# Performance work log

Hardware: AMD Instinct MI355X
Metric: run time of the kernel (lower is better)

The kernel has to match this reference:

```python
import jax, jax.numpy as jnp
import numpy as np

EPS = 1e-5
SCALE = 1.0 / np.float32(np.sqrt(64.0))  # 1/sqrt(d_Q)


def layernorm(x):
    # fresh nn.LayerNorm each call: gamma=1, beta=0
    m = jnp.mean(x, axis=-1, keepdims=True)
    v = jnp.mean((x - m) ** 2, axis=-1, keepdims=True)
    return (x - m) * jax.lax.rsqrt(v + EPS)


def setup_inputs() -> dict:
    key = jax.random.key(0)
    ks = jax.random.split(key, 8)
    B, S, D, H, F = 32, 512, 256, 64, 256
    w = 0.05
    return {
        "x": jax.random.normal(ks[0], (B, S, D), jnp.float32),
        "mask": jax.random.randint(ks[1], (B, 6, S, S), 0, 2).astype(jnp.int32),
        "Wq": jax.random.normal(ks[2], (6, D, H), jnp.float32) * w,
        "Wk": jax.random.normal(ks[3], (6, D, H), jnp.float32) * w,
        "Wv": jax.random.normal(ks[4], (6, D, H), jnp.float32) * w,
        "Wfc": jax.random.normal(ks[5], (6, H, D), jnp.float32) * w,
        "W1": jax.random.normal(ks[6], (D, F), jnp.float32) * w,
        "W2": jax.random.normal(ks[7], (F, D), jnp.float32) * w,
    }


def reference(x, mask, Wq, Wk, Wv, Wfc, W1, W2):
    m = mask.astype(bool)                                   # [B,6,S,S]
    # batched over the 6 relation branches (r axis)
    Q = jnp.einsum('bsd,rdh->brsh', x, Wq)                  # [B,6,S,64]
    K = jnp.einsum('bsd,rdh->brsh', x, Wk)
    V = jnp.einsum('bsd,rdh->brsh', x, Wv)
    score = jnp.einsum('brsh,brth->brst', Q, K) * SCALE     # [B,6,S,S]
    score = jnp.where(m, jnp.float32(-1e9), score)
    attn = jax.nn.softmax(score, axis=-1)
    attn = jnp.where(m, jnp.float32(0.0), attn)             # post-softmax zeroing
    ctx = jnp.einsum('brst,brth->brsh', attn, V)            # [B,6,S,64]
    proj = jnp.einsum('brsh,rhd->brsd', ctx, Wfc)           # [B,6,S,256]
    branch = layernorm(proj + x[:, None, :, :])             # residual + fresh LN per branch
    s = jnp.sum(branch, axis=1)                             # sum of 6 branches [B,S,256]
    ffn = jnp.maximum(jnp.einsum('bsd,df->bsf', s, W1), 0.0)
    ffn = jnp.einsum('bsf,fd->bsd', ffn, W2)
    return layernorm(ffn + s)
```

## Files before the change

kernel.cpp:

```cpp
#include <hip/hip_runtime.h>
#include <hip/hip_bf16.h>

#define BB 32
#define RR 6
#define SS 512
#define DD 256
#define HH 64
#define FF 256

typedef short  short8 __attribute__((ext_vector_type(8)));
typedef short  short4v __attribute__((ext_vector_type(4)));
typedef float  f32x4  __attribute__((ext_vector_type(4)));
typedef unsigned short ushort_t;
typedef unsigned int   uint_t;

__device__ __forceinline__ ushort_t f2bf(float f) {
    __hip_bfloat16 b = __float2bfloat16(f);
    return __builtin_bit_cast(ushort_t, b);
}
__device__ __forceinline__ float bf2f(ushort_t u) {
    return __bfloat162float(__builtin_bit_cast(__hip_bfloat16, u));
}

__global__ __launch_bounds__(256) void convert_all_kernel(
        const float* __restrict__ x,
        const float* __restrict__ Wq, const float* __restrict__ Wk, const float* __restrict__ Wv,
        const float* __restrict__ Wfc, const float* __restrict__ W1, const float* __restrict__ W2,
        ushort_t* __restrict__ xb, ushort_t* __restrict__ wT, ushort_t* __restrict__ w1T,
        ushort_t* __restrict__ w2T, ushort_t* __restrict__ wfcT) {
    int bid = blockIdx.x;
    if (bid < 4096) {
        int gid = bid * 256 + threadIdx.x;
        float4 fv = ((const float4*)x)[gid];
        short4v o;
        o[0] = (short)f2bf(fv.x); o[1] = (short)f2bf(fv.y);
        o[2] = (short)f2bf(fv.z); o[3] = (short)f2bf(fv.w);
        *(short4v*)(xb + (size_t)gid * 4) = o;
        return;
    }
    int gid = (bid - 4096) * 256 + threadIdx.x;
    if (gid < 294912) {
        int n = gid >> 8, d = gid & 255;
        int r = n / 192, rem = n % 192;
        int which = rem >> 6, h = rem & 63;
        const float* W = which == 0 ? Wq : which == 1 ? Wk : Wv;
        wT[gid] = f2bf(W[(size_t)r * DD * HH + (size_t)d * HH + h]);
    } else if (gid < 360448) {
        int gg = gid - 294912;
        int f = gg >> 8, d = gg & 255;
        w1T[gg] = f2bf(W1[(size_t)d * FF + f]);
    } else if (gid < 425984) {
        int gg = gid - 360448;
        int d = gg >> 8, f = gg & 255;
        w2T[gg] = f2bf(W2[(size_t)f * DD + d]);
    } else {
        int gg = gid - 425984;
        int n = gg >> 6, h = gg & 63;
        int r = n >> 8, d = n & 255;
        wfcT[gg] = f2bf(Wfc[((size_t)r * HH + h) * DD + d]);
    }
}

__global__ __launch_bounds__(256) void qkv_mfma_kernel(
        const ushort_t* __restrict__ xb, const ushort_t* __restrict__ wT,
        ushort_t* __restrict__ q, ushort_t* __restrict__ k, ushort_t* __restrict__ v) {
    int bid = blockIdx.x;
    int id = (bid & 7) * 288 + (bid >> 3);
    int rt = id / 18, cw = id % 18;
    int r = cw / 3, which = cw % 3;

    int tid = threadIdx.x;
    int wv = tid >> 6, l = tid & 63;
    int wr = wv >> 1, wc = wv & 1;
    int g = l >> 4, lc = l & 15;

    const ushort_t* Arow = xb + ((size_t)(rt * 128 + wr * 64 + lc)) * DD + g * 8;
    const ushort_t* Brow = wT + ((size_t)(cw * 64 + wc * 32 + lc)) * DD + g * 8;

    f32x4 acc[4][2] = {};
    #pragma unroll 4
    for (int ks = 0; ks < 8; ++ks) {
        short8 af[4], bf[2];
        #pragma unroll
        for (int m = 0; m < 4; ++m)
            af[m] = *(const short8*)(Arow + (size_t)m * 16 * DD + ks * 32);
        #pragma unroll
        for (int n = 0; n < 2; ++n)
            bf[n] = *(const short8*)(Brow + (size_t)n * 16 * DD + ks * 32);
        #pragma unroll
        for (int m = 0; m < 4; ++m)
            #pragma unroll
            for (int n = 0; n < 2; ++n)
                acc[m][n] = __builtin_amdgcn_mfma_f32_16x16x32_bf16(af[m], bf[n], acc[m][n], 0, 0, 0);
    }

    ushort_t* outb = which == 0 ? q : which == 1 ? k : v;
    #pragma unroll
    for (int m = 0; m < 4; ++m) {
        #pragma unroll
        for (int reg = 0; reg < 4; ++reg) {
            int grow = rt * 128 + wr * 64 + m * 16 + g * 4 + reg;
            int orow = ((grow >> 9) * RR + r) * SS + (grow & (SS - 1));
            #pragma unroll
            for (int n = 0; n < 2; ++n)
                outb[(size_t)orow * HH + wc * 32 + n * 16 + lc] = f2bf(acc[m][n][reg]);
        }
    }
}

__global__ __launch_bounds__(256) void attn_mfma_kernel(
        const ushort_t* __restrict__ q, const ushort_t* __restrict__ k,
        const ushort_t* __restrict__ v, const int* __restrict__ mask,
        ushort_t* __restrict__ ctx) {
    int wg = blockIdx.x;
    int id = (wg & 7) * 192 + (wg >> 3);
    int br = id >> 3, qt = id & 7;

    __shared__ ushort_t K_lds[64 * 72];
    __shared__ ushort_t VT_lds[64 * 66];
    __shared__ ushort_t P_lds[4][16 * 72];

    int tid = threadIdx.x;
    int wv = tid >> 6, l = tid & 63;
    int g = l >> 4, lc = l & 15;

    int q0 = qt * 64 + wv * 16;
    const size_t base_kv = (size_t)br * SS * HH;

    short8 qf[2];
    #pragma unroll
    for (int kk = 0; kk < 2; ++kk)
        qf[kk] = *(const short8*)(q + ((size_t)br * SS + q0 + lc) * HH + kk * 32 + g * 8);

    f32x4 O[4] = {{0,0,0,0},{0,0,0,0},{0,0,0,0},{0,0,0,0}};
    float lrun[4] = {0.f, 0.f, 0.f, 0.f};

    const int* mb = mask + ((size_t)br * SS + q0) * SS;

    for (int t0 = 0; t0 < SS; t0 += 64) {
        __syncthreads();
        for (int c = tid; c < 512; c += 256) {
            int t = c >> 3, c8 = (c & 7) * 8;
            *(short8*)&K_lds[t * 72 + c8] =
                *(const short8*)(k + base_kv + (size_t)(t0 + t) * HH + c8);
        }
        {
            int h = tid & 63, tseg = tid >> 6;
            #pragma unroll
            for (int jj = 0; jj < 8; ++jj) {
                int t = tseg * 16 + jj * 2;
                uint_t p0 = v[base_kv + (size_t)(t0 + t) * HH + h];
                uint_t p1 = v[base_kv + (size_t)(t0 + t + 1) * HH + h];
                *(uint_t*)&VT_lds[h * 66 + t] = p0 | (p1 << 16);
            }
        }
        __syncthreads();

        f32x4 S[4];
        #pragma unroll
        for (int tc = 0; tc < 4; ++tc) {
            f32x4 c = {0, 0, 0, 0};
            #pragma unroll
            for (int kk = 0; kk < 2; ++kk) {
                short8 bf = *(const short8*)&K_lds[(tc * 16 + lc) * 72 + kk * 32 + g * 8];
                c = __builtin_amdgcn_mfma_f32_16x16x32_bf16(qf[kk], bf, c, 0, 0, 0);
            }
            S[tc] = c;
        }

        float psum[4] = {0.f, 0.f, 0.f, 0.f};
        ushort_t* Pw = P_lds[wv];
        #pragma unroll
        for (int tc = 0; tc < 4; ++tc)
            #pragma unroll
            for (int reg = 0; reg < 4; ++reg) {
                int qrow = 4 * g + reg;
                int mv = mb[(size_t)qrow * SS + t0 + tc * 16 + lc];
                float p = mv ? 0.f : __expf(S[tc][reg] * 0.125f);
                psum[reg] += p;
                Pw[(4 * g + reg) * 72 + tc * 16 + lc] = f2bf(p);
            }
        #pragma unroll
        for (int reg = 0; reg < 4; ++reg) {
            float ps = psum[reg];
            ps += __shfl_xor(ps, 1, 64);
            ps += __shfl_xor(ps, 2, 64);
            ps += __shfl_xor(ps, 4, 64);
            ps += __shfl_xor(ps, 8, 64);
            lrun[reg] += ps;
        }
        asm volatile("s_waitcnt lgkmcnt(0)" ::: "memory");

        #pragma unroll
        for (int ts = 0; ts < 2; ++ts) {
            short8 pa = *(const short8*)&Pw[lc * 72 + ts * 32 + g * 8];
            #pragma unroll
            for (int hb = 0; hb < 4; ++hb) {
                short8 vbf = *(const short8*)&VT_lds[(hb * 16 + lc) * 66 + ts * 32 + g * 8];
                O[hb] = __builtin_amdgcn_mfma_f32_16x16x32_bf16(pa, vbf, O[hb], 0, 0, 0);
            }
        }
    }

    ushort_t* cb = ctx + ((size_t)br * SS + q0) * HH;
    #pragma unroll
    for (int reg = 0; reg < 4; ++reg) {
        float inv = lrun[reg] > 0.f ? 1.f / lrun[reg] : 0.f;
        #pragma unroll
        for (int hb = 0; hb < 4; ++hb)
            cb[(size_t)(4 * g + reg) * HH + hb * 16 + lc] = f2bf(O[hb][reg] * inv);
    }
}

__global__ __launch_bounds__(256) void fused_tail_kernel(
        const ushort_t* __restrict__ ctx, const ushort_t* __restrict__ wfcT,
        const float* __restrict__ x, const ushort_t* __restrict__ w1T,
        const ushort_t* __restrict__ w2T, float* __restrict__ out) {
    int bid = blockIdx.x;
    int rt = (bid & 7) * 64 + (bid >> 3);
    int b = rt >> 4, s0 = (rt & 15) * 32;

    int tid = threadIdx.x;
    int wv = tid >> 6, l = tid & 63;
    int wr = wv >> 1, wc = wv & 1;
    int g = l >> 4, lc = l & 15;

    __shared__ ushort_t s_lds[32 * 264];
    __shared__ ushort_t h_lds[32 * 264];
    __shared__ float red_s[RR][32][2];
    __shared__ float red_q[RR][32][2];

    float xres[8][4];
    #pragma unroll
    for (int hb = 0; hb < 8; ++hb)
        #pragma unroll
        for (int reg = 0; reg < 4; ++reg)
            xres[hb][reg] = x[((size_t)b * SS + s0 + wr * 16 + g * 4 + reg) * DD
                              + wc * 128 + hb * 16 + lc];

    float acc_ln[8][4] = {};

    for (int r = 0; r < RR; ++r) {
        const ushort_t* Abase = ctx + (((size_t)b * RR + r) * SS + s0 + wr * 16 + lc) * HH + g * 8;
        const ushort_t* Bbase = wfcT + ((size_t)r * 256 + wc * 128 + lc) * HH + g * 8;
        f32x4 acc[8] = {};
        #pragma unroll
        for (int ks = 0; ks < 2; ++ks) {
            short8 af = *(const short8*)(Abase + ks * 32);
            #pragma unroll
            for (int hb = 0; hb < 8; ++hb) {
                short8 bf = *(const short8*)(Bbase + (size_t)hb * 16 * HH + ks * 32);
                acc[hb] = __builtin_amdgcn_mfma_f32_16x16x32_bf16(af, bf, acc[hb], 0, 0, 0);
            }
        }

        float vals[8][4];
        float psum[4] = {0, 0, 0, 0}, psq[4] = {0, 0, 0, 0};
        #pragma unroll
        for (int hb = 0; hb < 8; ++hb)
            #pragma unroll
            for (int reg = 0; reg < 4; ++reg) {
                float vv = acc[hb][reg] + xres[hb][reg];
                vals[hb][reg] = vv;
                psum[reg] += vv;
                psq[reg]  += vv * vv;
            }
        #pragma unroll
        for (int reg = 0; reg < 4; ++reg) {
            #pragma unroll
            for (int off = 1; off <= 8; off <<= 1) {
                psum[reg] += __shfl_xor(psum[reg], off, 64);
                psq[reg]  += __shfl_xor(psq[reg],  off, 64);
            }
        }
        if (lc == 0) {
            #pragma unroll
            for (int reg = 0; reg < 4; ++reg) {
                int row = wr * 16 + g * 4 + reg;
                red_s[r][row][wc] = psum[reg];
                red_q[r][row][wc] = psq[reg];
            }
        }
        __syncthreads();
        #pragma unroll
        for (int reg = 0; reg < 4; ++reg) {
            int row = wr * 16 + g * 4 + reg;
            float sum = red_s[r][row][0] + red_s[r][row][1];
            float sq  = red_q[r][row][0] + red_q[r][row][1];
            float mean = sum * (1.f / 256.f);
            float var  = sq * (1.f / 256.f) - mean * mean;
            float inv  = rsqrtf(var + 1e-5f);
            #pragma unroll
            for (int hb = 0; hb < 8; ++hb)
                acc_ln[hb][reg] += (vals[hb][reg] - mean) * inv;
        }
    }

    #pragma unroll
    for (int hb = 0; hb < 8; ++hb)
        #pragma unroll
        for (int reg = 0; reg < 4; ++reg) {
            int row = wr * 16 + g * 4 + reg;
            int col = wc * 128 + hb * 16 + lc;
            s_lds[row * 264 + col] = f2bf(acc_ln[hb][reg]);
        }
    __syncthreads();

    f32x4 acc1[8] = {};
    #pragma unroll
    for (int ks = 0; ks < 8; ++ks) {
        short8 af = *(const short8*)&s_lds[(wr * 16 + lc) * 264 + ks * 32 + g * 8];
        #pragma unroll
        for (int hb = 0; hb < 8; ++hb) {
            short8 bf = *(const short8*)(w1T + (size_t)(wc * 128 + hb * 16 + lc) * DD + ks * 32 + g * 8);
            acc1[hb] = __builtin_amdgcn_mfma_f32_16x16x32_bf16(af, bf, acc1[hb], 0, 0, 0);
        }
    }
    #pragma unroll
    for (int hb = 0; hb < 8; ++hb)
        #pragma unroll
        for (int reg = 0; reg < 4; ++reg) {
            int row = wr * 16 + g * 4 + reg;
            int col = wc * 128 + hb * 16 + lc;
            h_lds[row * 264 + col] = f2bf(fmaxf(acc1[hb][reg], 0.f));
        }
    __syncthreads();

    f32x4 acc2[8] = {};
    #pragma unroll
    for (int ks = 0; ks < 8; ++ks) {
        short8 af = *(const short8*)&h_lds[(wr * 16 + lc) * 264 + ks * 32 + g * 8];
        #pragma unroll
        for (int hb = 0; hb < 8; ++hb) {
            short8 bf = *(const short8*)(w2T + (size_t)(wc * 128 + hb * 16 + lc) * FF + ks * 32 + g * 8);
            acc2[hb] = __builtin_amdgcn_mfma_f32_16x16x32_bf16(af, bf, acc2[hb], 0, 0, 0);
        }
    }

    float vals[8][4];
    float psum[4] = {0, 0, 0, 0}, psq[4] = {0, 0, 0, 0};
    #pragma unroll
    for (int hb = 0; hb < 8; ++hb)
        #pragma unroll
        for (int reg = 0; reg < 4; ++reg) {
            int row = wr * 16 + g * 4 + reg;
            int col = wc * 128 + hb * 16 + lc;
            float vv = acc2[hb][reg] + bf2f(s_lds[row * 264 + col]);
            vals[hb][reg] = vv;
            psum[reg] += vv;
            psq[reg]  += vv * vv;
        }
    #pragma unroll
    for (int reg = 0; reg < 4; ++reg) {
        #pragma unroll
        for (int off = 1; off <= 8; off <<= 1) {
            psum[reg] += __shfl_xor(psum[reg], off, 64);
            psq[reg]  += __shfl_xor(psq[reg],  off, 64);
        }
    }
    if (lc == 0) {
        #pragma unroll
        for (int reg = 0; reg < 4; ++reg) {
            int row = wr * 16 + g * 4 + reg;
            red_s[0][row][wc] = psum[reg];
            red_q[0][row][wc] = psq[reg];
        }
    }
    __syncthreads();
    #pragma unroll
    for (int reg = 0; reg < 4; ++reg) {
        int row = wr * 16 + g * 4 + reg;
        float sum = red_s[0][row][0] + red_s[0][row][1];
        float sq  = red_q[0][row][0] + red_q[0][row][1];
        float mean = sum * (1.f / 256.f);
        float var  = sq * (1.f / 256.f) - mean * mean;
        float inv  = rsqrtf(var + 1e-5f);
        #pragma unroll
        for (int hb = 0; hb < 8; ++hb) {
            int col = wc * 128 + hb * 16 + lc;
            out[((size_t)rt * 32 + row) * DD + col] = (vals[hb][reg] - mean) * inv;
        }
    }
}

extern "C" void kernel_launch(void* const* d_in, const int* in_sizes, int n_in,
                              void* d_out, int out_size, void* d_ws, size_t ws_size,
                              hipStream_t stream) {
    const float* x    = (const float*)d_in[0];
    const int*   mask = (const int*)  d_in[1];
    const float* Wq   = (const float*)d_in[2];
    const float* Wk   = (const float*)d_in[3];
    const float* Wv   = (const float*)d_in[4];
    const float* Wfc  = (const float*)d_in[5];
    const float* W1   = (const float*)d_in[6];
    const float* W2   = (const float*)d_in[7];
    float* out = (float*)d_out;

    const size_t QKV = (size_t)BB * RR * SS * HH;
    const size_t BSD = (size_t)BB * SS * DD;
    ushort_t* qb  = (ushort_t*)d_ws;
    ushort_t* kb  = qb + QKV;
    ushort_t* vb  = kb + QKV;
    ushort_t* ctx = vb + QKV;
    ushort_t* xb  = ctx + QKV;
    ushort_t* wT  = xb + BSD;
    ushort_t* w1T = wT + (size_t)1152 * 256;
    ushort_t* w2T = w1T + 65536;
    ushort_t* wfcT = w2T + 65536;

    convert_all_kernel<<<6144, 256, 0, stream>>>(x, Wq, Wk, Wv, Wfc, W1, W2,
                                                 xb, wT, w1T, w2T, wfcT);
    qkv_mfma_kernel  <<<2304, 256, 0, stream>>>(xb, wT, qb, kb, vb);
    attn_mfma_kernel <<<BB * RR * 8, 256, 0, stream>>>(qb, kb, vb, mask, ctx);
    fused_tail_kernel<<<512, 256, 0, stream>>>(ctx, wfcT, x, w1T, w2T, out);
}
```

Baseline: 192.5 us.

## Split fused tail into branch-parallel projection and separate FFN kernel

The single tail kernel looped over all six relation branches per 32-row tile with only 512 blocks. It is now split into a projection+LayerNorm kernel that handles two branches per block across 1536 blocks, writing three fp32 partial sums to a workspace buffer. A new FFN kernel reads and adds the three partials before running the two GEMMs and the final LayerNorm. This trades extra global memory traffic (three fp32 BSD buffers written and read) and one extra launch for more parallelism in the projection stage.

```diff
diff --git a/kernel.cpp b/kernel.cpp
--- a/kernel.cpp
+++ b/kernel.cpp
@@ -212,12 +212,12 @@
     }
 }
 
-__global__ __launch_bounds__(256) void fused_tail_kernel(
+__global__ __launch_bounds__(256) void proj2_kernel(
         const ushort_t* __restrict__ ctx, const ushort_t* __restrict__ wfcT,
-        const float* __restrict__ x, const ushort_t* __restrict__ w1T,
-        const ushort_t* __restrict__ w2T, float* __restrict__ out) {
+        const float* __restrict__ x, float* __restrict__ pbuf) {
     int bid = blockIdx.x;
-    int rt = (bid & 7) * 64 + (bid >> 3);
+    int id = (bid & 7) * 192 + (bid >> 3);
+    int grp = id / 512, rt = id % 512;
     int b = rt >> 4, s0 = (rt & 15) * 32;
 
     int tid = threadIdx.x;
@@ -225,10 +225,8 @@
     int wr = wv >> 1, wc = wv & 1;
     int g = l >> 4, lc = l & 15;
 
-    __shared__ ushort_t s_lds[32 * 264];
-    __shared__ ushort_t h_lds[32 * 264];
-    __shared__ float red_s[RR][32][2];
-    __shared__ float red_q[RR][32][2];
+    __shared__ float red_s[2][32][2];
+    __shared__ float red_q[2][32][2];
 
     float xres[8][4];
     #pragma unroll
@@ -240,7 +238,9 @@
 
     float acc_ln[8][4] = {};
 
-    for (int r = 0; r < RR; ++r) {
+    #pragma unroll
+    for (int rr = 0; rr < 2; ++rr) {
+        int r = grp * 2 + rr;
         const ushort_t* Abase = ctx + (((size_t)b * RR + r) * SS + s0 + wr * 16 + lc) * HH + g * 8;
         const ushort_t* Bbase = wfcT + ((size_t)r * 256 + wc * 128 + lc) * HH + g * 8;
         f32x4 acc[8] = {};
@@ -277,16 +277,16 @@
             #pragma unroll
             for (int reg = 0; reg < 4; ++reg) {
                 int row = wr * 16 + g * 4 + reg;
-                red_s[r][row][wc] = psum[reg];
-                red_q[r][row][wc] = psq[reg];
+                red_s[rr][row][wc] = psum[reg];
+                red_q[rr][row][wc] = psq[reg];
             }
         }
         __syncthreads();
         #pragma unroll
         for (int reg = 0; reg < 4; ++reg) {
             int row = wr * 16 + g * 4 + reg;
-            float sum = red_s[r][row][0] + red_s[r][row][1];
-            float sq  = red_q[r][row][0] + red_q[r][row][1];
+            float sum = red_s[rr][row][0] + red_s[rr][row][1];
+            float sq  = red_q[rr][row][0] + red_q[rr][row][1];
             float mean = sum * (1.f / 256.f);
             float var  = sq * (1.f / 256.f) - mean * mean;
             float inv  = rsqrtf(var + 1e-5f);
@@ -296,14 +296,50 @@
         }
     }
 
+    float* outp = pbuf + (size_t)grp * ((size_t)BB * SS * DD);
     #pragma unroll
     for (int hb = 0; hb < 8; ++hb)
         #pragma unroll
         for (int reg = 0; reg < 4; ++reg) {
             int row = wr * 16 + g * 4 + reg;
             int col = wc * 128 + hb * 16 + lc;
-            s_lds[row * 264 + col] = f2bf(acc_ln[hb][reg]);
-        }
+            outp[((size_t)rt * 32 + row) * DD + col] = acc_ln[hb][reg];
+        }
+}
+
+__global__ __launch_bounds__(256) void ffn_kernel(
+        const float* __restrict__ pbuf, const ushort_t* __restrict__ w1T,
+        const ushort_t* __restrict__ w2T, float* __restrict__ out) {
+    int bid = blockIdx.x;
+    int rt = (bid & 7) * 64 + (bid >> 3);
+    int tid = threadIdx.x;
+    int wv = tid >> 6, l = tid & 63;
+    int wr = wv >> 1, wc = wv & 1;
+    int g = l >> 4, lc = l & 15;
+
+    __shared__ ushort_t s_lds[32 * 264];
+    __shared__ ushort_t h_lds[32 * 264];
+    __shared__ float red_s[32][2];
+    __shared__ float red_q[32][2];
+
+    const size_t BSD = (size_t)BB * SS * DD;
+    const float* p0 = pbuf;
+    const float* p1 = pbuf + BSD;
+    const float* p2 = pbuf + 2 * BSD;
+
+    for (int c = tid; c < 2048; c += 256) {
+        int row = c >> 6, q4 = c & 63;
+        size_t idx = ((size_t)rt * 32 + row) * DD + q4 * 4;
+        float4 a = *(const float4*)(p0 + idx);
+        float4 bq = *(const float4*)(p1 + idx);
+        float4 cq = *(const float4*)(p2 + idx);
+        short4v o;
+        o[0] = (short)f2bf(a.x + bq.x + cq.x);
+        o[1] = (short)f2bf(a.y + bq.y + cq.y);
+        o[2] = (short)f2bf(a.z + bq.z + cq.z);
+        o[3] = (short)f2bf(a.w + bq.w + cq.w);
+        *(short4v*)&s_lds[row * 264 + q4 * 4] = o;
+    }
     __syncthreads();
 
     f32x4 acc1[8] = {};
@@ -362,16 +398,16 @@
         #pragma unroll
         for (int reg = 0; reg < 4; ++reg) {
             int row = wr * 16 + g * 4 + reg;
-            red_s[0][row][wc] = psum[reg];
-            red_q[0][row][wc] = psq[reg];
+            red_s[row][wc] = psum[reg];
+            red_q[row][wc] = psq[reg];
         }
     }
     __syncthreads();
     #pragma unroll
     for (int reg = 0; reg < 4; ++reg) {
         int row = wr * 16 + g * 4 + reg;
-        float sum = red_s[0][row][0] + red_s[0][row][1];
-        float sq  = red_q[0][row][0] + red_q[0][row][1];
+        float sum = red_s[row][0] + red_s[row][1];
+        float sq  = red_q[row][0] + red_q[row][1];
         float mean = sum * (1.f / 256.f);
         float var  = sq * (1.f / 256.f) - mean * mean;
         float inv  = rsqrtf(var + 1e-5f);
@@ -407,10 +443,12 @@
     ushort_t* w1T = wT + (size_t)1152 * 256;
     ushort_t* w2T = w1T + 65536;
     ushort_t* wfcT = w2T + 65536;
+    float* pbuf = (float*)(wfcT + (size_t)RR * 256 * 64);
 
     convert_all_kernel<<<6144, 256, 0, stream>>>(x, Wq, Wk, Wv, Wfc, W1, W2,
                                                  xb, wT, w1T, w2T, wfcT);
     qkv_mfma_kernel  <<<2304, 256, 0, stream>>>(xb, wT, qb, kb, vb);
     attn_mfma_kernel <<<BB * RR * 8, 256, 0, stream>>>(qb, kb, vb, mask, ctx);
-    fused_tail_kernel<<<512, 256, 0, stream>>>(ctx, wfcT, x, w1T, w2T, out);
-}
+    proj2_kernel     <<<1536, 256, 0, stream>>>(ctx, wfcT, x, pbuf);
+    ffn_kernel       <<<512, 256, 0, stream>>>(pbuf, w1T, w2T, out);
+}
```

Measured after the change: 208.7 us. 8.4% more time.
